# Performance work log

Hardware: AMD Instinct MI355X
Metric: run time of the kernel (lower is better)

Reference implementation:

```python
import jax, jax.numpy as jnp
import numpy as np

BETA = 0.9
THR = 1.0
B, T, F, H = 64, 256, 1024, 512

# snntorch heaviside spike with ATan surrogate gradient (alpha=2.0, snntorch default)
@jax.custom_vjp
def spike_fn(u):
    return (u > 0).astype(u.dtype)

def _spike_fwd(u):
    return spike_fn(u), u

def _spike_bwd(u, g):
    alpha = 2.0
    grad = (alpha / 2.0) / (1.0 + (jnp.pi / 2.0 * alpha * u) ** 2)
    return (g * grad,)

spike_fn.defvjp(_spike_fwd, _spike_bwd)


def setup_inputs() -> dict:
    key = jax.random.key(0)
    ks = jax.random.split(key, 12)
    s = 0.05
    return {
        "f_f": jax.random.normal(ks[0], (B, T, F), dtype=jnp.float32),
        "seq_len": jnp.full((B,), T, dtype=jnp.int64),
        "Wf": jax.random.normal(ks[1], (H, F), dtype=jnp.float32) * s,
        "bf": jnp.zeros((H,), jnp.float32),
        "W1": jax.random.normal(ks[2], (H, H), dtype=jnp.float32) * s,
        "b1": jnp.zeros((H,), jnp.float32),
        "W2": jax.random.normal(ks[3], (H, H), dtype=jnp.float32) * s,
        "b2": jnp.zeros((H,), jnp.float32),
        "Mw1": jax.random.normal(ks[4], (512, H), dtype=jnp.float32) * s,
        "Mb1": jnp.zeros((512,), jnp.float32),
        "Mw2": jax.random.normal(ks[5], (32, 512), dtype=jnp.float32) * s,
        "Mb2": jnp.zeros((32,), jnp.float32),
        "Mw3": jax.random.normal(ks[6], (1, 32), dtype=jnp.float32) * s,
        "Mb3": jnp.zeros((1,), jnp.float32),
    }


def _forward(f_f, Wf, bf, W1, b1, W2, b2, Mw1, Mb1, Mw2, Mb2, Mw3, Mb3):
    h = f_f @ Wf.T + bf            # [B,T,H] fc_f
    x1 = h @ W1.T + b1             # layer-1 linear drive precomputed (state-independent)

    def step(carry, x1_t):
        m1, m2 = carry
        # snntorch Leaky (subtract reset): reset from previous mem's spike
        r1 = spike_fn(m1 - THR)
        m1 = BETA * m1 + x1_t - r1 * THR
        s1 = spike_fn(m1 - THR)
        x2 = s1 @ W2.T + b2        # layer-2 linear on spikes (dropout=identity, eval)
        r2 = spike_fn(m2 - THR)
        m2 = BETA * m2 + x2 - r2 * THR
        s2 = spike_fn(m2 - THR)
        return (m1, m2), s2

    init = (jnp.zeros((B, H), h.dtype), jnp.zeros((B, H), h.dtype))
    _, spk = jax.lax.scan(step, init, jnp.swapaxes(x1, 0, 1))  # [T,B,H]
    spk = jnp.swapaxes(spk, 0, 1)                              # [B,T,H]

    z = jax.nn.relu(spk @ Mw1.T + Mb1)
    z = z @ Mw2.T + Mb2
    logits = jax.nn.sigmoid((z @ Mw3.T + Mb3).squeeze(-1))     # [B,T]

    # filter: top-(seq_len//16 + 1) mean per clip; seq_len == T for all clips
    k = T // 16 + 1
    topv, _ = jax.lax.top_k(logits, k)
    return jnp.mean(topv, axis=-1)                             # [B]


def reference(f_f, seq_len, Wf, bf, W1, b1, W2, b2, Mw1, Mb1, Mw2, Mb2, Mw3, Mb3):
    return _forward(f_f, Wf, bf, W1, b1, W2, b2, Mw1, Mb1, Mw2, Mb2, Mw3, Mb3)
```

## Files before the change

kernel.cpp:

```cpp
#include <hip/hip_runtime.h>
#include <math.h>

#define BETA 0.9f
#define THR 1.0f

constexpr int B_ = 64, T_ = 256, F_ = 1024, H_ = 512;
constexpr int M_ = B_ * T_;

typedef float f32x4 __attribute__((ext_vector_type(4)));
typedef short short8 __attribute__((ext_vector_type(8)));
typedef _Float16 half8 __attribute__((ext_vector_type(8)));
typedef unsigned short us4 __attribute__((ext_vector_type(4)));
typedef unsigned short us8 __attribute__((ext_vector_type(8)));
typedef unsigned short ushort_t;

static __device__ __forceinline__ unsigned short f2bf(float x) {
    unsigned b = __builtin_bit_cast(unsigned, x);
    unsigned r = (b + 0x7FFFu + ((b >> 16) & 1u)) >> 16;
    return (unsigned short)r;
}
static __device__ __forceinline__ float bf2f(unsigned short u) {
    unsigned v = ((unsigned)u) << 16;
    return __builtin_bit_cast(float, v);
}
static __device__ __forceinline__ unsigned short f2h(float x) {
    _Float16 h = (_Float16)x;
    return __builtin_bit_cast(unsigned short, h);
}
static __device__ __forceinline__ float h2f(unsigned short u) {
    return (float)__builtin_bit_cast(_Float16, u);
}
static __device__ __forceinline__ int swz(int r) {
    return ((r >> 2) & 3) ^ (r & 3);
}

#define GLDS(srcp, dstp)                                                      \
    __builtin_amdgcn_global_load_lds(                                         \
        (const __attribute__((address_space(1))) unsigned int*)(srcp),        \
        (__attribute__((address_space(3))) unsigned int*)(dstp), 16, 0, 0)

template <int AF32>
__global__ __launch_bounds__(256, 2) void gemm_scan(
    const void* __restrict__ Asrc, const ushort_t* __restrict__ Bp,
    const float* __restrict__ bias, ushort_t* __restrict__ Sout, int K) {
    constexpr int BUF = 20480;
    __shared__ ushort_t lds[2 * BUF];

    const int tid = threadIdx.x;
    const int w = tid >> 6, l = tid & 63;
    const int flat = blockIdx.y * gridDim.x + blockIdx.x;
    const int clip = ((flat >> 6) << 3) | (flat & 7);
    const int strip = (flat >> 3) & 7;
    const int n0 = strip * 64;
    const int m0 = clip * 256;

    f32x4 acc[4][4];
#pragma unroll
    for (int mi = 0; mi < 4; ++mi)
#pragma unroll
        for (int ni = 0; ni < 4; ++ni) acc[mi][ni] = (f32x4){0.f, 0.f, 0.f, 0.f};

    const int c0 = l >> 4;
    const int schunk = (l & 7) ^ ((l >> 3) & 7);

    f32x4 areg[8][2];

    auto stageB = [&](int buf, int k0) {
#pragma unroll
        for (int j = 0; j < 2; ++j) {
            const int seg = w * 2 + j;
            const int r = seg * 8 + (l >> 3);
            GLDS((const ushort_t*)Bp + (size_t)(n0 + r) * K + k0 + schunk * 8,
                 &lds[buf + 16384 + seg * 512]);
        }
    };
    auto stageA16 = [&](int buf, int k0) {
#pragma unroll
        for (int j = 0; j < 8; ++j) {
            const int seg = w * 8 + j;
            const int r = seg * 8 + (l >> 3);
            GLDS((const ushort_t*)Asrc + (size_t)(m0 + r) * K + k0 + schunk * 8,
                 &lds[buf + seg * 512]);
        }
    };
    auto loadA32 = [&](int k0) {
#pragma unroll
        for (int j = 0; j < 8; ++j) {
            const int r = j * 32 + w * 8 + (l >> 3);
            const float* src =
                (const float*)Asrc + (size_t)(m0 + r) * K + k0 + (l & 7) * 8;
            areg[j][0] = *(const f32x4*)src;
            areg[j][1] = *(const f32x4*)(src + 4);
        }
    };
    auto writeA32 = [&](int buf) {
#pragma unroll
        for (int j = 0; j < 8; ++j) {
            const int r = j * 32 + w * 8 + (l >> 3);
            us8 hv;
#pragma unroll
            for (int e = 0; e < 4; ++e) {
                hv[e] = f2h(areg[j][0][e]);
                hv[e + 4] = f2h(areg[j][1][e]);
            }
            const int pos = (l & 7) ^ (r & 7);
            *(us8*)&lds[buf + r * 64 + pos * 8] = hv;
        }
    };

    const int nt = K / 64;
    if constexpr (AF32) {
        loadA32(0);
        writeA32(0);
    } else {
        stageA16(0, 0);
    }
    stageB(0, 0);

    for (int t = 0; t < nt; ++t) {
        const int cur = (t & 1) * BUF;
        const int nxt = BUF - cur;
        __syncthreads();
        const bool more = (t + 1 < nt);
        if (more) {
            if constexpr (AF32) {
                loadA32((t + 1) * 64);
                __builtin_amdgcn_sched_barrier(0);
                stageB(nxt, (t + 1) * 64);
            } else {
                stageA16(nxt, (t + 1) * 64);
                stageB(nxt, (t + 1) * 64);
            }
        }

#pragma unroll
        for (int kh = 0; kh < 2; ++kh) {
            half8 aa[4], bb[4];
            const int q = kh * 4 + c0;
#pragma unroll
            for (int mi = 0; mi < 4; ++mi) {
                const int r = w * 64 + mi * 16 + (l & 15);
                const int off = cur + r * 64 + ((q ^ (l & 7)) * 8);
                aa[mi] = __builtin_bit_cast(half8, *(const short8*)&lds[off]);
            }
#pragma unroll
            for (int ni = 0; ni < 4; ++ni) {
                const int r = ni * 16 + (l & 15);
                const int off = cur + 16384 + r * 64 + ((q ^ (l & 7)) * 8);
                bb[ni] = __builtin_bit_cast(half8, *(const short8*)&lds[off]);
            }
#pragma unroll
            for (int mi = 0; mi < 4; ++mi)
#pragma unroll
                for (int ni = 0; ni < 4; ++ni)
                    acc[mi][ni] = __builtin_amdgcn_mfma_f32_16x16x32_f16(
                        aa[mi], bb[ni], acc[mi][ni], 0, 0, 0);
        }

        if constexpr (AF32) {
            if (more) {
                __builtin_amdgcn_sched_barrier(0);
                writeA32(nxt);
            }
        }
    }

    float bv[4];
#pragma unroll
    for (int ni = 0; ni < 4; ++ni) bv[ni] = bias[n0 + ni * 16 + (l & 15)];
#pragma unroll
    for (int mi = 0; mi < 4; ++mi) {
        const int t0 = w * 64 + mi * 16 + ((l >> 4) << 2);
#pragma unroll
        for (int ni = 0; ni < 4; ++ni) {
            const int h = ni * 16 + (l & 15);
#pragma unroll
            for (int r = 0; r < 4; ++r)
                lds[(t0 + r) * 66 + h] = f2h(acc[mi][ni][r] + bv[ni]);
        }
    }
    __syncthreads();

    if (tid < 64) {
        const int h = tid;
        ushort_t* sp = Sout + (size_t)m0 * 512 + n0 + h;
        float m = 0.f;
#pragma unroll 4
        for (int t = 0; t < T_; ++t) {
            const float xv = h2f(lds[t * 66 + h]);
            const float r = (m - THR > 0.f) ? THR : 0.f;
            m = BETA * m + xv - r;
            sp[(size_t)t * 512] = (m - THR > 0.f) ? (ushort_t)0x3C00 : (ushort_t)0;
        }
    }
}

__global__ __launch_bounds__(256) void gemm_mil(
    const ushort_t* __restrict__ Ap, const ushort_t* __restrict__ Bp,
    const float* __restrict__ bias, const float* __restrict__ Uv,
    float* __restrict__ part, int N, int K) {
    constexpr int BUF = 16384;
    __shared__ ushort_t lds[2 * BUF];

    const int tid = threadIdx.x;
    const int w = tid >> 6, l = tid & 63;
    const int flat = blockIdx.y * gridDim.x + blockIdx.x;
    const int mt = ((flat >> 5) << 3) | (flat & 7);
    const int st = (flat >> 3) & 3;
    const int n0 = st * 128;
    const int m0 = mt * 128;
    const int wr = w >> 1, wc = w & 1;

    f32x4 acc[4][4];
#pragma unroll
    for (int mi = 0; mi < 4; ++mi)
#pragma unroll
        for (int ni = 0; ni < 4; ++ni) acc[mi][ni] = (f32x4){0.f, 0.f, 0.f, 0.f};

    const int c0 = l >> 4;
    const int schunk = (l & 7) ^ ((l >> 3) & 7);

    auto stage = [&](int buf, int k0) {
#pragma unroll
        for (int j = 0; j < 8; ++j) {
            const int g = w * 8 + j;
            const int seg = g & 15;
            const int r = seg * 8 + (l >> 3);
            const ushort_t* pl = (g < 16) ? Ap : Bp;
            const int rb = (g < 16) ? m0 : n0;
            GLDS(pl + (size_t)(rb + r) * K + k0 + schunk * 8,
                 &lds[buf + g * 512]);
        }
    };

    const int nt = K / 64;
    stage(0, 0);
    for (int t = 0; t < nt; ++t) {
        const int cur = (t & 1) * BUF;
        const int nxt = BUF - cur;
        __syncthreads();
        if (t + 1 < nt) stage(nxt, (t + 1) * 64);

#pragma unroll
        for (int kh = 0; kh < 2; ++kh) {
            half8 aa[4], bb[4];
            const int q = kh * 4 + c0;
#pragma unroll
            for (int mi = 0; mi < 4; ++mi) {
                const int r = wr * 64 + mi * 16 + (l & 15);
                const int off = cur + r * 64 + ((q ^ (l & 7)) * 8);
                aa[mi] = __builtin_bit_cast(half8, *(const short8*)&lds[off]);
            }
#pragma unroll
            for (int ni = 0; ni < 4; ++ni) {
                const int r = wc * 64 + ni * 16 + (l & 15);
                const int off = cur + 8192 + r * 64 + ((q ^ (l & 7)) * 8);
                bb[ni] = __builtin_bit_cast(half8, *(const short8*)&lds[off]);
            }
#pragma unroll
            for (int mi = 0; mi < 4; ++mi)
#pragma unroll
                for (int ni = 0; ni < 4; ++ni)
                    acc[mi][ni] = __builtin_amdgcn_mfma_f32_16x16x32_f16(
                        aa[mi], bb[ni], acc[mi][ni], 0, 0, 0);
        }
    }

    float bv[4], uc[4];
#pragma unroll
    for (int ni = 0; ni < 4; ++ni) {
        const int col = n0 + wc * 64 + ni * 16 + (l & 15);
        bv[ni] = bias[col];
        uc[ni] = Uv[col];
    }
    const int strip = (n0 >> 6) + wc;
#pragma unroll
    for (int mi = 0; mi < 4; ++mi) {
        float p[4];
#pragma unroll
        for (int r = 0; r < 4; ++r) {
            float s = 0.f;
#pragma unroll
            for (int ni = 0; ni < 4; ++ni)
                s += fmaxf(acc[mi][ni][r] + bv[ni], 0.f) * uc[ni];
            p[r] = s;
        }
#pragma unroll
        for (int off = 1; off <= 8; off <<= 1)
#pragma unroll
            for (int r = 0; r < 4; ++r) p[r] += __shfl_xor(p[r], off);
        if ((l & 15) == 0) {
            const int row0 = m0 + wr * 64 + mi * 16 + ((l >> 4) << 2);
#pragma unroll
            for (int r = 0; r < 4; ++r)
                part[(size_t)strip * M_ + row0 + r] = p[r];
        }
    }
}

__global__ __launch_bounds__(256) void gemm_bf16_wc(
    const ushort_t* __restrict__ Ah, const ushort_t* __restrict__ Al,
    const ushort_t* __restrict__ Bh, const ushort_t* __restrict__ Bl,
    ushort_t* __restrict__ Cout, int N, int K) {
    __shared__ ushort_t lds[4 * 4096];

    const int tid = threadIdx.x;
    const int w = tid >> 6, l = tid & 63;
    const int nwg = gridDim.x * gridDim.y;
    const int flat = blockIdx.y * gridDim.x + blockIdx.x;
    const int wg = (flat & 7) * (nwg >> 3) + (flat >> 3);
    const int n0 = (wg % gridDim.x) * 128;
    const int m0 = (wg / gridDim.x) * 128;
    const int wr = w >> 1, wc = w & 1;

    f32x4 acc[4][4];
#pragma unroll
    for (int mi = 0; mi < 4; ++mi)
#pragma unroll
        for (int ni = 0; ni < 4; ++ni) acc[mi][ni] = (f32x4){0.f, 0.f, 0.f, 0.f};

    const int c0 = l >> 4;
    for (int k0 = 0; k0 < K; k0 += 32) {
        __syncthreads();
#pragma unroll
        for (int j = 0; j < 8; ++j) {
            const int g = w * 8 + j;
            const int p = g >> 3, seg = g & 7;
            const int r = seg * 16 + (l >> 2);
            const int ch = (l & 3) ^ swz(r);
            const ushort_t* pl = (p == 0) ? Ah : (p == 1) ? Al : (p == 2) ? Bh : Bl;
            const int rb = (p < 2) ? m0 : n0;
            GLDS(pl + (size_t)(rb + r) * K + k0 + ch * 8,
                 &lds[p * 4096 + seg * 512]);
        }
        __syncthreads();

        short8 ah[4], al[4], bh[4], bl[4];
#pragma unroll
        for (int mi = 0; mi < 4; ++mi) {
            const int r = wr * 64 + mi * 16 + (l & 15);
            const int off = r * 32 + ((c0 ^ swz(r)) * 8);
            ah[mi] = *(const short8*)&lds[off];
            al[mi] = *(const short8*)&lds[4096 + off];
        }
#pragma unroll
        for (int ni = 0; ni < 4; ++ni) {
            const int r = wc * 64 + ni * 16 + (l & 15);
            const int off = r * 32 + ((c0 ^ swz(r)) * 8);
            bh[ni] = *(const short8*)&lds[8192 + off];
            bl[ni] = *(const short8*)&lds[12288 + off];
        }
#pragma unroll
        for (int mi = 0; mi < 4; ++mi)
#pragma unroll
            for (int ni = 0; ni < 4; ++ni) {
                acc[mi][ni] = __builtin_amdgcn_mfma_f32_16x16x32_bf16(
                    ah[mi], bh[ni], acc[mi][ni], 0, 0, 0);
                acc[mi][ni] = __builtin_amdgcn_mfma_f32_16x16x32_bf16(
                    ah[mi], bl[ni], acc[mi][ni], 0, 0, 0);
                acc[mi][ni] = __builtin_amdgcn_mfma_f32_16x16x32_bf16(
                    al[mi], bh[ni], acc[mi][ni], 0, 0, 0);
            }
    }

#pragma unroll
    for (int ni = 0; ni < 4; ++ni) {
        const int col = n0 + wc * 64 + ni * 16 + (l & 15);
#pragma unroll
        for (int mi = 0; mi < 4; ++mi) {
            const int row0 = m0 + wr * 64 + mi * 16 + ((l >> 4) << 2);
#pragma unroll
            for (int r = 0; r < 4; ++r)
                Cout[(size_t)(row0 + r) * N + col] = f2h(acc[mi][ni][r]);
        }
    }
}

__global__ __launch_bounds__(256) void prep_small(
    const float* __restrict__ W1, const float* __restrict__ W2,
    const float* __restrict__ Mw1, const float* __restrict__ bfv,
    const float* __restrict__ b1, const float* __restrict__ Mw2,
    const float* __restrict__ Mb2, const float* __restrict__ Mw3,
    const float* __restrict__ Mb3, const float* __restrict__ Wf,
    ushort_t* __restrict__ w1h, ushort_t* __restrict__ w1l,
    ushort_t* __restrict__ w2f, ushort_t* __restrict__ m1f,
    float* __restrict__ bc, float* __restrict__ uc,
    ushort_t* __restrict__ wfTh, ushort_t* __restrict__ wfTl) {
    __shared__ float tile[32][33];
    const int blk = blockIdx.x;
    const int tid = threadIdx.x;
    if (blk < 256) {
        const int i = blk * 256 + tid;
        f32x4 v = ((const f32x4*)W1)[i];
        us4 h, ll;
#pragma unroll
        for (int e = 0; e < 4; ++e) {
            const unsigned short hb = f2bf(v[e]);
            h[e] = hb;
            ll[e] = f2bf(v[e] - bf2f(hb));
        }
        ((us4*)w1h)[i] = h;
        ((us4*)w1l)[i] = ll;
    } else if (blk < 512) {
        const int i = (blk - 256) * 256 + tid;
        f32x4 v = ((const f32x4*)W2)[i];
        us4 h;
#pragma unroll
        for (int e = 0; e < 4; ++e) h[e] = f2h(v[e]);
        ((us4*)w2f)[i] = h;
    } else if (blk < 768) {
        const int i = (blk - 512) * 256 + tid;
        f32x4 v = ((const f32x4*)Mw1)[i];
        us4 h;
#pragma unroll
        for (int e = 0; e < 4; ++e) h[e] = f2h(v[e]);
        ((us4*)m1f)[i] = h;
    } else if (blk < 896) {
        const int w = tid >> 6, l = tid & 63;
        const int j = (blk - 768) * 4 + w;
        const float* row = W1 + (size_t)j * 512;
        float a = 0.f;
#pragma unroll
        for (int i = 0; i < 8; ++i) a += row[l + i * 64] * bfv[l + i * 64];
#pragma unroll
        for (int off = 32; off >= 1; off >>= 1) a += __shfl_xor(a, off);
        if (l == 0) bc[j] = a + b1[j];
    } else if (blk < 898) {
        const int j = (blk - 896) * 256 + tid;
        float a = 0.f;
        for (int i = 0; i < 32; ++i) a += Mw3[i] * Mw2[(size_t)i * 512 + j];
        uc[j] = a;
        if (j == 0) {
            float c = Mb3[0];
            for (int i = 0; i < 32; ++i) c += Mw3[i] * Mb2[i];
            uc[512] = c;
        }
    } else {
        const int idx = blk - 898;
        const int k0 = (idx & 31) * 32;
        const int i0 = (idx >> 5) * 32;
        const int tx = tid & 31;
        const int ty = tid >> 5;
#pragma unroll
        for (int e = 0; e < 4; ++e) {
            const int i = ty + e * 8;
            tile[i][tx] = Wf[(size_t)(i0 + i) * 1024 + k0 + tx];
        }
        __syncthreads();
#pragma unroll
        for (int e = 0; e < 4; ++e) {
            const int kk = ty + e * 8;
            const float v = tile[tx][kk];
            const unsigned short h = f2bf(v);
            wfTh[(size_t)(k0 + kk) * 512 + i0 + tx] = h;
            wfTl[(size_t)(k0 + kk) * 512 + i0 + tx] = f2bf(v - bf2f(h));
        }
    }
}

__global__ __launch_bounds__(64) void tail_topk(const float* __restrict__ part,
                                                const float* __restrict__ uc,
                                                float* __restrict__ out) {
    const int b = blockIdx.x;
    const int lane = threadIdx.x;
    const float c = uc[512];
    float v[4];
#pragma unroll
    for (int i = 0; i < 4; ++i) {
        const int row = b * T_ + lane + i * 64;
        float a = 0.f;
#pragma unroll
        for (int s = 0; s < 8; ++s) a += part[(size_t)s * M_ + row];
        v[i] = a + c;
    }
    float sum = 0.f;
    for (int iter = 0; iter < 17; ++iter) {
        float mv = v[0];
        int mslot = 0;
#pragma unroll
        for (int i = 1; i < 4; ++i)
            if (v[i] > mv) { mv = v[i]; mslot = i; }
        float bv = mv;
        int bl = lane, bs = mslot;
#pragma unroll
        for (int off = 32; off >= 1; off >>= 1) {
            const float ov = __shfl_xor(bv, off);
            const int ol = __shfl_xor(bl, off);
            const int os = __shfl_xor(bs, off);
            if (ov > bv || (ov == bv && ol < bl)) { bv = ov; bl = ol; bs = os; }
        }
        sum += 1.f / (1.f + expf(-bv));
        if (lane == bl) v[bs] = -1e30f;
    }
    if (lane == 0) out[b] = sum * (1.f / 17.f);
}

extern "C" void kernel_launch(void* const* d_in, const int* in_sizes, int n_in,
                              void* d_out, int out_size, void* d_ws, size_t ws_size,
                              hipStream_t stream) {
    const float* f_f = (const float*)d_in[0];
    const float* Wf  = (const float*)d_in[2];
    const float* bf  = (const float*)d_in[3];
    const float* W1  = (const float*)d_in[4];
    const float* b1  = (const float*)d_in[5];
    const float* W2  = (const float*)d_in[6];
    const float* b2  = (const float*)d_in[7];
    const float* Mw1 = (const float*)d_in[8];
    const float* Mb1 = (const float*)d_in[9];
    const float* Mw2 = (const float*)d_in[10];
    const float* Mb2 = (const float*)d_in[11];
    const float* Mw3 = (const float*)d_in[12];
    const float* Mb3 = (const float*)d_in[13];
    float* out = (float*)d_out;

    char* ws = (char*)d_ws;
    const size_t NE = (size_t)M_ * H_;
    ushort_t* sbuf1 = (ushort_t*)ws;
    ushort_t* sbuf2 = sbuf1 + NE;
    ushort_t* w1h = sbuf2 + NE;
    ushort_t* w1l = w1h + 262144;
    ushort_t* w2f = w1l + 262144;
    ushort_t* m1f = w2f + 262144;
    ushort_t* wfTh = m1f + 262144;
    ushort_t* wfTl = wfTh + 524288;
    ushort_t* wcf = wfTl + 524288;
    float* bc = (float*)(wcf + 524288);
    float* uc = bc + 512;
    float* part = uc + 513 + 63;

    const dim3 blk(256);

    prep_small<<<dim3(1410), blk, 0, stream>>>(W1, W2, Mw1, bf, b1, Mw2, Mb2,
                                               Mw3, Mb3, Wf, w1h, w1l, w2f,
                                               m1f, bc, uc, wfTh, wfTl);

    gemm_bf16_wc<<<dim3(8, 4), blk, 0, stream>>>(w1h, w1l, wfTh, wfTl, wcf,
                                                 1024, 512);
    gemm_scan<1><<<dim3(8, 64), blk, 0, stream>>>(f_f, wcf, bc, sbuf1, 1024);
    gemm_scan<0><<<dim3(8, 64), blk, 0, stream>>>(sbuf1, w2f, b2, sbuf2, 512);
    gemm_mil<<<dim3(4, 128), blk, 0, stream>>>(sbuf2, m1f, Mb1, uc, part,
                                               512, 512);
    tail_topk<<<dim3(B_), dim3(64), 0, stream>>>(part, uc, out);
}
```

Baseline: 114.3 us.

## Run gemm_scan with 512-thread blocks, halving per-wave tile and registers

Doubles the gemm_scan block to 8 waves, each owning 32 rows instead of 64, so the accumulator and A-staging registers are halved and launch bounds request 4 blocks per CU. It also drops the sched_barriers around the fp32 A loads and the fp16 convert-and-store. The aim is more waves resident to hide the global loads and LDS latency. In exchange, every wave re-reads the full B tile from LDS, so B fragment traffic per MFMA doubles. Dropping the barriers lets the compiler reorder the loads, which may hurt the intended overlap.

```diff
diff --git a/kernel.cpp b/kernel.cpp
--- a/kernel.cpp
+++ b/kernel.cpp
@@ -40,7 +40,7 @@
         (__attribute__((address_space(3))) unsigned int*)(dstp), 16, 0, 0)
 
 template <int AF32>
-__global__ __launch_bounds__(256, 2) void gemm_scan(
+__global__ __launch_bounds__(512, 4) void gemm_scan(
     const void* __restrict__ Asrc, const ushort_t* __restrict__ Bp,
     const float* __restrict__ bias, ushort_t* __restrict__ Sout, int K) {
     constexpr int BUF = 20480;
@@ -54,30 +54,26 @@
     const int n0 = strip * 64;
     const int m0 = clip * 256;
 
-    f32x4 acc[4][4];
-#pragma unroll
-    for (int mi = 0; mi < 4; ++mi)
+    f32x4 acc[2][4];
+#pragma unroll
+    for (int mi = 0; mi < 2; ++mi)
 #pragma unroll
         for (int ni = 0; ni < 4; ++ni) acc[mi][ni] = (f32x4){0.f, 0.f, 0.f, 0.f};
 
     const int c0 = l >> 4;
     const int schunk = (l & 7) ^ ((l >> 3) & 7);
 
-    f32x4 areg[8][2];
+    f32x4 areg[4][2];
 
     auto stageB = [&](int buf, int k0) {
-#pragma unroll
-        for (int j = 0; j < 2; ++j) {
-            const int seg = w * 2 + j;
-            const int r = seg * 8 + (l >> 3);
-            GLDS((const ushort_t*)Bp + (size_t)(n0 + r) * K + k0 + schunk * 8,
-                 &lds[buf + 16384 + seg * 512]);
-        }
+        const int r = w * 8 + (l >> 3);
+        GLDS(Bp + (size_t)(n0 + r) * K + k0 + schunk * 8,
+             &lds[buf + 16384 + w * 512]);
     };
     auto stageA16 = [&](int buf, int k0) {
 #pragma unroll
-        for (int j = 0; j < 8; ++j) {
-            const int seg = w * 8 + j;
+        for (int j = 0; j < 4; ++j) {
+            const int seg = w * 4 + j;
             const int r = seg * 8 + (l >> 3);
             GLDS((const ushort_t*)Asrc + (size_t)(m0 + r) * K + k0 + schunk * 8,
                  &lds[buf + seg * 512]);
@@ -85,25 +81,25 @@
     };
     auto loadA32 = [&](int k0) {
 #pragma unroll
-        for (int j = 0; j < 8; ++j) {
-            const int r = j * 32 + w * 8 + (l >> 3);
+        for (int j = 0; j < 4; ++j) {
+            const int r = j * 64 + (tid >> 3);
             const float* src =
-                (const float*)Asrc + (size_t)(m0 + r) * K + k0 + (l & 7) * 8;
+                (const float*)Asrc + (size_t)(m0 + r) * K + k0 + (tid & 7) * 8;
             areg[j][0] = *(const f32x4*)src;
             areg[j][1] = *(const f32x4*)(src + 4);
         }
     };
     auto writeA32 = [&](int buf) {
 #pragma unroll
-        for (int j = 0; j < 8; ++j) {
-            const int r = j * 32 + w * 8 + (l >> 3);
+        for (int j = 0; j < 4; ++j) {
+            const int r = j * 64 + (tid >> 3);
             us8 hv;
 #pragma unroll
             for (int e = 0; e < 4; ++e) {
                 hv[e] = f2h(areg[j][0][e]);
                 hv[e + 4] = f2h(areg[j][1][e]);
             }
-            const int pos = (l & 7) ^ (r & 7);
+            const int pos = (tid & 7) ^ (r & 7);
             *(us8*)&lds[buf + r * 64 + pos * 8] = hv;
         }
     };
@@ -125,7 +121,6 @@
         if (more) {
             if constexpr (AF32) {
                 loadA32((t + 1) * 64);
-                __builtin_amdgcn_sched_barrier(0);
                 stageB(nxt, (t + 1) * 64);
             } else {
                 stageA16(nxt, (t + 1) * 64);
@@ -135,11 +130,11 @@
 
 #pragma unroll
         for (int kh = 0; kh < 2; ++kh) {
-            half8 aa[4], bb[4];
+            half8 aa[2], bb[4];
             const int q = kh * 4 + c0;
 #pragma unroll
-            for (int mi = 0; mi < 4; ++mi) {
-                const int r = w * 64 + mi * 16 + (l & 15);
+            for (int mi = 0; mi < 2; ++mi) {
+                const int r = w * 32 + mi * 16 + (l & 15);
                 const int off = cur + r * 64 + ((q ^ (l & 7)) * 8);
                 aa[mi] = __builtin_bit_cast(half8, *(const short8*)&lds[off]);
             }
@@ -150,7 +145,7 @@
                 bb[ni] = __builtin_bit_cast(half8, *(const short8*)&lds[off]);
             }
 #pragma unroll
-            for (int mi = 0; mi < 4; ++mi)
+            for (int mi = 0; mi < 2; ++mi)
 #pragma unroll
                 for (int ni = 0; ni < 4; ++ni)
                     acc[mi][ni] = __builtin_amdgcn_mfma_f32_16x16x32_f16(
@@ -158,10 +153,7 @@
         }
 
         if constexpr (AF32) {
-            if (more) {
-                __builtin_amdgcn_sched_barrier(0);
-                writeA32(nxt);
-            }
+            if (more) writeA32(nxt);
         }
     }
 
@@ -169,8 +161,8 @@
 #pragma unroll
     for (int ni = 0; ni < 4; ++ni) bv[ni] = bias[n0 + ni * 16 + (l & 15)];
 #pragma unroll
-    for (int mi = 0; mi < 4; ++mi) {
-        const int t0 = w * 64 + mi * 16 + ((l >> 4) << 2);
+    for (int mi = 0; mi < 2; ++mi) {
+        const int t0 = w * 32 + mi * 16 + ((l >> 4) << 2);
 #pragma unroll
         for (int ni = 0; ni < 4; ++ni) {
             const int h = ni * 16 + (l & 15);
@@ -536,8 +528,10 @@
 
     gemm_bf16_wc<<<dim3(8, 4), blk, 0, stream>>>(w1h, w1l, wfTh, wfTl, wcf,
                                                  1024, 512);
-    gemm_scan<1><<<dim3(8, 64), blk, 0, stream>>>(f_f, wcf, bc, sbuf1, 1024);
-    gemm_scan<0><<<dim3(8, 64), blk, 0, stream>>>(sbuf1, w2f, b2, sbuf2, 512);
+    gemm_scan<1><<<dim3(8, 64), dim3(512), 0, stream>>>(f_f, wcf, bc, sbuf1,
+                                                        1024);
+    gemm_scan<0><<<dim3(8, 64), dim3(512), 0, stream>>>(sbuf1, w2f, b2, sbuf2,
+                                                        512);
     gemm_mil<<<dim3(4, 128), blk, 0, stream>>>(sbuf2, m1f, Mb1, uc, part,
                                                512, 512);
     tail_topk<<<dim3(B_), dim3(64), 0, stream>>>(part, uc, out);
```

Result: no change. 112.3 us (-1.8%).
